# Optimization experiments

Hardware: AMD Instinct MI355X
Metric: run time of the kernel (lower is better)

Reference implementation:

```python
import jax, jax.numpy as jnp
import numpy as np

INPUT_SIZE = 695 + 2 * 406 + 84  # 1591
HIDDEN = 1024
NUM_LAYERS = 2
B, T = 8, 2048


def _make_linear(key, fan_in, fan_out, forget_bias):
    kw, kb = jax.random.split(key)
    bound = 1.0 / np.sqrt(fan_in)
    W = jax.random.uniform(kw, (fan_in, fan_out), minval=-bound, maxval=bound, dtype=jnp.float32)
    b = jax.random.uniform(kb, (fan_out,), minval=-bound, maxval=bound, dtype=jnp.float32)
    H = fan_out // 3
    b = b.at[H:2 * H].set(forget_bias)  # init_input_passthrough: forget-gate bias = 6.0
    return W, b


def setup_inputs() -> dict:
    key = jax.random.key(0)
    k1, k2, k3, k4, k5 = jax.random.split(key, 5)
    prev_actions = jax.random.uniform(k1, (B, T, 695), dtype=jnp.float32)
    states = jax.random.uniform(k2, (B, T, 812), dtype=jnp.float32)
    metadata = jax.random.uniform(k3, (B, T, 84), dtype=jnp.float32)
    W1, b1 = _make_linear(k4, INPUT_SIZE, 3 * HIDDEN, 6.0)
    W2, b2 = _make_linear(k5, HIDDEN, 3 * HIDDEN, 6.0)
    return {"prev_actions": prev_actions, "states": states, "metadata": metadata,
            "W1": W1, "b1": b1, "W2": W2, "b2": b2}


def forget_mult(f, z):
    # c_t = f_t * z_t + (1 - f_t) * c_{t-1}, c_0 = 0; parallel (log-depth) scan over time.
    a = 1.0 - f          # decay
    b = f * z            # input term
    def combine(c1, c2):
        a1, b1 = c1
        a2, b2 = c2
        return a1 * a2, a2 * b1 + b2
    _, c = jax.lax.associative_scan(combine, (a, b), axis=-2)
    return c


def qrnn_layer(x, W, b):
    y = jnp.einsum('btd,dh->bth', x, W) + b          # [B,T,3H]
    Z, Fg, O = jnp.split(y, 3, axis=-1)
    C = forget_mult(jax.nn.sigmoid(Fg), jax.nn.relu(Z))  # [B,T,H]
    out = jax.nn.sigmoid(O) * C
    return out, C[..., -1, :]


def reference(prev_actions, states, metadata, W1, b1, W2, b2):
    x = jnp.concatenate([prev_actions, states, metadata], axis=-1)  # [B,T,1591]
    hs = []
    for W, b in ((W1, b1), (W2, b2)):
        x, h_last = qrnn_layer(x, W, b)
        hs.append(h_last)
    h = jnp.stack(hs, axis=-2)  # [B, num_layers, H]
    return x, h
```

## Files before the change

kernel.cpp:

```cpp
#include <hip/hip_runtime.h>

typedef unsigned short u16;
typedef unsigned int   u32;
typedef __attribute__((ext_vector_type(8))) short bf16x8;
typedef __attribute__((ext_vector_type(4))) float f32x4;

#define B_ 8
#define T_ 2048
#define M_ 16384
#define N_ 3072
#define H_ 1024
#define L_ 64
#define NC_ 32

__device__ __forceinline__ u16 f2bf(float f) {
    union { float f; unsigned u; } v; v.f = f;
    unsigned r = v.u + 0x7FFFu + ((v.u >> 16) & 1u);
    return (u16)(r >> 16);
}
__device__ __forceinline__ float bf2f(u16 s) {
    union { unsigned u; float f; } v; v.u = ((unsigned)s) << 16;
    return v.f;
}
__device__ __forceinline__ float sigm(float x) {
    return 1.f / (1.f + __expf(-x));
}

__device__ __forceinline__ void gload_lds16(const void* g, void* l) {
    __builtin_amdgcn_global_load_lds(
        (const __attribute__((address_space(1))) unsigned int*)g,
        (__attribute__((address_space(3))) unsigned int*)l,
        16, 0, 0);
}

__global__ void concat_cast(const float* __restrict__ pa, const float* __restrict__ st,
                            const float* __restrict__ md, u16* __restrict__ x) {
    const int m = blockIdx.x;
    const float* pam = pa + (size_t)m * 695;
    const float* stm = st + (size_t)m * 812;
    const float* mdm = md + (size_t)m * 84;
    u16* xm = x + (size_t)m * 1600;
    for (int d = threadIdx.x; d < 1600; d += 256) {
        float v;
        if (d < 695)       v = pam[d];
        else if (d < 1507) v = stm[d - 695];
        else if (d < 1591) v = mdm[d - 1507];
        else               v = 0.f;
        xm[d] = f2bf(v);
    }
}

__global__ void wtrans(const float* __restrict__ W, u16* __restrict__ Wt, int K, int Kp) {
    __shared__ float tile[32][33];
    const int n0 = blockIdx.x << 5;
    const int k0 = blockIdx.y << 5;
    const int tx = threadIdx.x & 31, ty = threadIdx.x >> 5;
    #pragma unroll
    for (int i = 0; i < 32; i += 8) {
        int k = k0 + ty + i;
        tile[ty + i][tx] = (k < K) ? W[(size_t)k * N_ + n0 + tx] : 0.f;
    }
    __syncthreads();
    #pragma unroll
    for (int i = 0; i < 32; i += 8) {
        int n = n0 + ty + i;
        Wt[(size_t)n * Kp + k0 + tx] = f2bf(tile[tx][ty + i]);
    }
}

__global__ __launch_bounds__(256, 2)
void gemm_bt(const u16* __restrict__ A, const u16* __restrict__ Bt,
             const float* __restrict__ bias, u16* __restrict__ Y, int Kp) {
    __shared__ u16 a_tile[128 * 32];
    __shared__ u16 b_tile[128 * 32];
    const int tid = threadIdx.x;
    const int w = tid >> 6, l = tid & 63;
    const int brow = blockIdx.y << 7, bcol = blockIdx.x << 7;
    const int wr = (w >> 1) << 6, wc = (w & 1) << 6;
    const int lr = l & 15, lk = (l >> 4) << 3;

    const int ra0 = (w << 4) + (l >> 2);
    const int kc  = (l & 3) << 3;
    const u16* ga = A  + (size_t)(brow + ra0) * Kp + kc;
    const u16* gb = Bt + (size_t)(bcol + ra0) * Kp + kc;
    u16* la = a_tile + (w << 4) * 32;
    u16* lb = b_tile + (w << 4) * 32;

    f32x4 acc[4][4] = {};

    for (int kk = 0; kk < Kp; kk += 32) {
        gload_lds16(ga + kk,                    la);
        gload_lds16(ga + kk + (size_t)64 * Kp,  la + 64 * 32);
        gload_lds16(gb + kk,                    lb);
        gload_lds16(gb + kk + (size_t)64 * Kp,  lb + 64 * 32);
        __syncthreads();

        bf16x8 af[4], bfr[4];
        #pragma unroll
        for (int mi = 0; mi < 4; ++mi)
            af[mi] = *reinterpret_cast<const bf16x8*>(&a_tile[(wr + mi * 16 + lr) * 32 + lk]);
        #pragma unroll
        for (int ni = 0; ni < 4; ++ni)
            bfr[ni] = *reinterpret_cast<const bf16x8*>(&b_tile[(wc + ni * 16 + lr) * 32 + lk]);
        #pragma unroll
        for (int mi = 0; mi < 4; ++mi)
            #pragma unroll
            for (int ni = 0; ni < 4; ++ni)
                acc[mi][ni] = __builtin_amdgcn_mfma_f32_16x16x32_bf16(af[mi], bfr[ni], acc[mi][ni], 0, 0, 0);
        __syncthreads();
    }

    const int row0 = (l >> 4) << 2;
    #pragma unroll
    for (int ni = 0; ni < 4; ++ni) {
        const int gc = bcol + wc + ni * 16 + lr;
        const float bv = bias[gc];
        #pragma unroll
        for (int mi = 0; mi < 4; ++mi) {
            #pragma unroll
            for (int j = 0; j < 4; ++j) {
                const int gr = brow + wr + mi * 16 + row0 + j;
                Y[(size_t)gr * N_ + gc] = f2bf(acc[mi][ni][j] + bv);
            }
        }
    }
}

__global__ void scan_p1(const u16* __restrict__ y, float* __restrict__ aprod,
                        float* __restrict__ cend) {
    const int hb = blockIdx.x & 1;
    const int chunk = (blockIdx.x >> 1) & (NC_ - 1);
    const int b = blockIdx.x >> 6;
    const int h = (hb << 9) + (threadIdx.x << 1);
    const u16* yb = y + ((size_t)b * T_ + (size_t)chunk * L_) * N_;
    float a0 = 1.f, a1 = 1.f, c0 = 0.f, c1 = 0.f;
    #pragma unroll 4
    for (int t = 0; t < L_; ++t) {
        const u32 zz = *reinterpret_cast<const u32*>(&yb[t * N_ + h]);
        const u32 ff = *reinterpret_cast<const u32*>(&yb[t * N_ + H_ + h]);
        const float f0 = sigm(bf2f((u16)ff));
        const float f1 = sigm(bf2f((u16)(ff >> 16)));
        const float z0 = fmaxf(bf2f((u16)zz), 0.f);
        const float z1 = fmaxf(bf2f((u16)(zz >> 16)), 0.f);
        c0 = f0 * z0 + (1.f - f0) * c0;  a0 *= (1.f - f0);
        c1 = f1 * z1 + (1.f - f1) * c1;  a1 *= (1.f - f1);
    }
    const size_t idx = ((size_t)b * NC_ + chunk) * H_ + h;
    *reinterpret_cast<float2*>(&aprod[idx]) = make_float2(a0, a1);
    *reinterpret_cast<float2*>(&cend[idx])  = make_float2(c0, c1);
}

__global__ void scan_p2(const float* __restrict__ aprod, const float* __restrict__ cend,
                        float* __restrict__ cin, float* __restrict__ hout, int layer) {
    const int b = blockIdx.x >> 2;
    const int h = ((blockIdx.x & 3) << 8) + threadIdx.x;
    float c = 0.f;
    #pragma unroll
    for (int k = 0; k < NC_; ++k) {
        const size_t idx = ((size_t)b * NC_ + k) * H_ + h;
        cin[idx] = c;
        c = aprod[idx] * c + cend[idx];
    }
    hout[(size_t)(((b << 1) + layer) << 10) + h] = c;
}

__global__ void scan_p3(const u16* __restrict__ y, const float* __restrict__ cin,
                        void* __restrict__ xout, int layer) {
    const int hb = blockIdx.x & 1;
    const int chunk = (blockIdx.x >> 1) & (NC_ - 1);
    const int b = blockIdx.x >> 6;
    const int h = (hb << 9) + (threadIdx.x << 1);
    const u16* yb = y + ((size_t)b * T_ + (size_t)chunk * L_) * N_;
    const size_t cidx = ((size_t)b * NC_ + chunk) * H_ + h;
    const float2 cv = *reinterpret_cast<const float2*>(&cin[cidx]);
    float c0 = cv.x, c1 = cv.y;
    u32*    xo_bf = (u32*)xout;
    float2* xo_f  = (float2*)xout;
    const size_t obase = ((size_t)b * T_ + (size_t)chunk * L_) * H_ + h;
    #pragma unroll 4
    for (int t = 0; t < L_; ++t) {
        const u32 zz = *reinterpret_cast<const u32*>(&yb[t * N_ + h]);
        const u32 ff = *reinterpret_cast<const u32*>(&yb[t * N_ + H_ + h]);
        const u32 oo = *reinterpret_cast<const u32*>(&yb[t * N_ + 2 * H_ + h]);
        const float f0 = sigm(bf2f((u16)ff));
        const float f1 = sigm(bf2f((u16)(ff >> 16)));
        const float z0 = fmaxf(bf2f((u16)zz), 0.f);
        const float z1 = fmaxf(bf2f((u16)(zz >> 16)), 0.f);
        c0 = f0 * z0 + (1.f - f0) * c0;
        c1 = f1 * z1 + (1.f - f1) * c1;
        const float o0 = sigm(bf2f((u16)oo)) * c0;
        const float o1 = sigm(bf2f((u16)(oo >> 16))) * c1;
        const size_t oi = obase + (size_t)t * H_;
        if (layer) xo_f[oi >> 1] = make_float2(o0, o1);
        else       xo_bf[oi >> 1] = (u32)f2bf(o0) | ((u32)f2bf(o1) << 16);
    }
}

extern "C" void kernel_launch(void* const* d_in, const int* in_sizes, int n_in,
                              void* d_out, int out_size, void* d_ws, size_t ws_size,
                              hipStream_t stream) {
    const float* pa = (const float*)d_in[0];
    const float* st = (const float*)d_in[1];
    const float* md = (const float*)d_in[2];
    const float* W1 = (const float*)d_in[3];
    const float* b1 = (const float*)d_in[4];
    const float* W2 = (const float*)d_in[5];
    const float* b2 = (const float*)d_in[6];
    float* out = (float*)d_out;

    char* ws = (char*)d_ws;
    const size_t y_bytes = (size_t)M_ * N_ * 2;
    const size_t x_bytes = (size_t)M_ * 1600 * 2;
    u16* y  = (u16*)ws;
    u16* x  = (u16*)(ws + y_bytes);
    u16* Wt = (u16*)(ws + y_bytes + x_bytes);
    char* scr = ws + y_bytes + (size_t)M_ * H_ * 2;
    const size_t sarr = (size_t)B_ * NC_ * H_ * 4;
    float* aprod = (float*)scr;
    float* cend  = (float*)(scr + sarr);
    float* cin   = (float*)(scr + 2 * sarr);

    float* hout = out + (size_t)M_ * H_;

    concat_cast<<<M_, 256, 0, stream>>>(pa, st, md, x);
    wtrans<<<dim3(N_ / 32, 50), 256, 0, stream>>>(W1, Wt, 1591, 1600);
    gemm_bt<<<dim3(N_ / 128, M_ / 128), 256, 0, stream>>>(x, Wt, b1, y, 1600);
    scan_p1<<<B_ * NC_ * 2, 256, 0, stream>>>(y, aprod, cend);
    scan_p2<<<32, 256, 0, stream>>>(aprod, cend, cin, hout, 0);
    scan_p3<<<B_ * NC_ * 2, 256, 0, stream>>>(y, cin, x, 0);

    wtrans<<<dim3(N_ / 32, 32), 256, 0, stream>>>(W2, Wt, 1024, 1024);
    gemm_bt<<<dim3(N_ / 128, M_ / 128), 256, 0, stream>>>(x, Wt, b2, y, 1024);
    scan_p1<<<B_ * NC_ * 2, 256, 0, stream>>>(y, aprod, cend);
    scan_p2<<<32, 256, 0, stream>>>(aprod, cend, cin, hout, 1);
    scan_p3<<<B_ * NC_ * 2, 256, 0, stream>>>(y, cin, out, 1);
}
```

Measured before the change: 480.3 us.

## Replace GEMM with 256x256 8-wave ping-pong pipelined kernel with swizzled LDS

Replaces the 128x128 single-buffered bf16 MFMA GEMM with a 256x256-tile, 512-thread kernel. It double-buffers 64-wide K slices in 128KB of LDS, splits each K step into four phases that overlap global-to-LDS loads with MFMA work using explicit waitcnt, barriers and setprio, and XOR-swizzles LDS slots to avoid bank conflicts. Blocks are remapped across 8 groups (likely for XCD locality). The goal is more data reuse per tile and hidden memory latency. In exchange it runs one block per CU with heavy register use, and Kp=1600 must divide evenly into 64-wide K tiles (25 of them).

```diff
diff --git a/kernel.cpp b/kernel.cpp
--- a/kernel.cpp
+++ b/kernel.cpp
@@ -68,62 +68,108 @@
     }
 }
 
-__global__ __launch_bounds__(256, 2)
-void gemm_bt(const u16* __restrict__ A, const u16* __restrict__ Bt,
-             const float* __restrict__ bias, u16* __restrict__ Y, int Kp) {
-    __shared__ u16 a_tile[128 * 32];
-    __shared__ u16 b_tile[128 * 32];
+#define AO_(c, kh) ((((c) << 2) + (kh)) << 13)
+#define BO_(c, kh) ((((c) << 2) + 2 + (kh)) << 13)
+
+__global__ __launch_bounds__(512, 1)
+void gemm8p(const u16* __restrict__ A, const u16* __restrict__ Bt,
+            const float* __restrict__ bias, u16* __restrict__ Y,
+            int Kp, int NK, int NBN) {
+    __shared__ u16 lds[65536];
     const int tid = threadIdx.x;
     const int w = tid >> 6, l = tid & 63;
-    const int brow = blockIdx.y << 7, bcol = blockIdx.x << 7;
-    const int wr = (w >> 1) << 6, wc = (w & 1) << 6;
-    const int lr = l & 15, lk = (l >> 4) << 3;
-
-    const int ra0 = (w << 4) + (l >> 2);
-    const int kc  = (l & 3) << 3;
-    const u16* ga = A  + (size_t)(brow + ra0) * Kp + kc;
-    const u16* gb = Bt + (size_t)(bcol + ra0) * Kp + kc;
-    u16* la = a_tile + (w << 4) * 32;
-    u16* lb = b_tile + (w << 4) * 32;
-
-    f32x4 acc[4][4] = {};
-
-    for (int kk = 0; kk < Kp; kk += 32) {
-        gload_lds16(ga + kk,                    la);
-        gload_lds16(ga + kk + (size_t)64 * Kp,  la + 64 * 32);
-        gload_lds16(gb + kk,                    lb);
-        gload_lds16(gb + kk + (size_t)64 * Kp,  lb + 64 * 32);
-        __syncthreads();
-
-        bf16x8 af[4], bfr[4];
-        #pragma unroll
-        for (int mi = 0; mi < 4; ++mi)
-            af[mi] = *reinterpret_cast<const bf16x8*>(&a_tile[(wr + mi * 16 + lr) * 32 + lk]);
-        #pragma unroll
-        for (int ni = 0; ni < 4; ++ni)
-            bfr[ni] = *reinterpret_cast<const bf16x8*>(&b_tile[(wc + ni * 16 + lr) * 32 + lk]);
-        #pragma unroll
-        for (int mi = 0; mi < 4; ++mi)
-            #pragma unroll
-            for (int ni = 0; ni < 4; ++ni)
-                acc[mi][ni] = __builtin_amdgcn_mfma_f32_16x16x32_bf16(af[mi], bfr[ni], acc[mi][ni], 0, 0, 0);
-        __syncthreads();
-    }
-
-    const int row0 = (l >> 4) << 2;
-    #pragma unroll
-    for (int ni = 0; ni < 4; ++ni) {
-        const int gc = bcol + wc + ni * 16 + lr;
+    const int wm = w >> 2, wn = w & 3;
+
+    const int cpx = gridDim.x >> 3;
+    const int xg = (blockIdx.x & 7) * cpx + (blockIdx.x >> 3);
+    const int bm = xg / NBN, bn = xg % NBN;
+    const int brow = bm << 8, bcol = bn << 8;
+
+    const int srow = l >> 2;
+    const int gslot = (l & 3) ^ (srow & 3);
+    const u16* ga = A  + (size_t)(brow + w * 32 + srow) * Kp + gslot * 8;
+    const u16* gb = Bt + (size_t)(bcol + w * 32 + srow) * Kp + gslot * 8;
+    const int ldst = w << 10;
+
+    const int fl = ((l & 15) << 5) + ((((l >> 4) ^ (l & 3)) & 3) << 3);
+    const int abase0 = (wm << 7) << 5;
+    const int bbase0 = (wn << 6) << 5;
+
+#define STG(OFF, gp, kt, kh) do {                                              \
+    gload_lds16((gp) + (size_t)(kt) * 64 + (kh) * 32, &lds[(OFF) + ldst]);     \
+    gload_lds16((gp) + 16 * (size_t)Kp + (size_t)(kt) * 64 + (kh) * 32,        \
+                &lds[(OFF) + ldst + 512]);                                     \
+} while (0)
+
+    f32x4 acc[8][4] = {};
+    bf16x8 bfr[4];
+
+    STG(AO_(0, 0), ga, 0, 0); STG(BO_(0, 0), gb, 0, 0);
+    STG(AO_(0, 1), ga, 0, 1); STG(BO_(0, 1), gb, 0, 1);
+    STG(AO_(1, 0), ga, 1, 0); STG(BO_(1, 0), gb, 1, 0);
+    asm volatile("s_waitcnt vmcnt(4)" ::: "memory");
+    __builtin_amdgcn_s_barrier();
+    asm volatile("" ::: "memory");
+
+#define PHASE(CH, KH, LOADB, STAGECODE, VMW) do {                              \
+    bf16x8 af[4];                                                              \
+    { const int ab = AO_(cur, KH) + abase0 + ((CH) << 11);                     \
+      _Pragma("unroll")                                                        \
+      for (int mf = 0; mf < 4; ++mf)                                           \
+          af[mf] = *reinterpret_cast<const bf16x8*>(&lds[ab + (mf << 9) + fl]);\
+    }                                                                          \
+    if (LOADB) {                                                               \
+        const int bb = BO_(cur, KH) + bbase0;                                  \
+        _Pragma("unroll")                                                      \
+        for (int nf = 0; nf < 4; ++nf)                                         \
+            bfr[nf] = *reinterpret_cast<const bf16x8*>(&lds[bb + (nf << 9) + fl]); \
+    }                                                                          \
+    STAGECODE;                                                                 \
+    if (VMW) asm volatile("s_waitcnt vmcnt(4)" ::: "memory");                  \
+    asm volatile("" ::: "memory");                                             \
+    __builtin_amdgcn_s_barrier();                                              \
+    asm volatile("s_waitcnt lgkmcnt(0)" ::: "memory");                         \
+    __builtin_amdgcn_sched_barrier(0);                                         \
+    __builtin_amdgcn_s_setprio(1);                                             \
+    _Pragma("unroll")                                                          \
+    for (int mf = 0; mf < 4; ++mf)                                             \
+        _Pragma("unroll")                                                      \
+        for (int nf = 0; nf < 4; ++nf)                                         \
+            acc[(CH) * 4 + mf][nf] = __builtin_amdgcn_mfma_f32_16x16x32_bf16(  \
+                af[mf], bfr[nf], acc[(CH) * 4 + mf][nf], 0, 0, 0);             \
+    __builtin_amdgcn_s_setprio(0);                                             \
+    __builtin_amdgcn_sched_barrier(0);                                         \
+    __builtin_amdgcn_s_barrier();                                              \
+    asm volatile("" ::: "memory");                                             \
+} while (0)
+
+    for (int kt = 0; kt < NK; ++kt) {
+        const int cur = kt & 1;
+        const int kn1 = (kt + 1 < NK) ? kt + 1 : kt;
+        const int kn2 = (kt + 2 < NK) ? kt + 2 : kt;
+        PHASE(0, 0, 1, { STG(AO_(cur ^ 1, 1), ga, kn1, 1); }, 0);
+        PHASE(1, 0, 0, { STG(BO_(cur ^ 1, 1), gb, kn1, 1); }, 1);
+        PHASE(0, 1, 1, { STG(AO_(cur, 0),     ga, kn2, 0); }, 0);
+        PHASE(1, 1, 0, { STG(BO_(cur, 0),     gb, kn2, 0); }, 1);
+    }
+
+    asm volatile("s_waitcnt vmcnt(0)" ::: "memory");
+
+    const int crow0 = brow + wm * 128 + ((l >> 4) << 2);
+    const int ccol0 = bcol + wn * 64 + (l & 15);
+    #pragma unroll
+    for (int nf = 0; nf < 4; ++nf) {
+        const int gc = ccol0 + nf * 16;
         const float bv = bias[gc];
         #pragma unroll
-        for (int mi = 0; mi < 4; ++mi) {
+        for (int mfi = 0; mfi < 8; ++mfi) {
             #pragma unroll
-            for (int j = 0; j < 4; ++j) {
-                const int gr = brow + wr + mi * 16 + row0 + j;
-                Y[(size_t)gr * N_ + gc] = f2bf(acc[mi][ni][j] + bv);
-            }
+            for (int j = 0; j < 4; ++j)
+                Y[(size_t)(crow0 + mfi * 16 + j) * N_ + gc] = f2bf(acc[mfi][nf][j] + bv);
         }
     }
+#undef PHASE
+#undef STG
 }
 
 __global__ void scan_p1(const u16* __restrict__ y, float* __restrict__ aprod,
@@ -222,15 +268,17 @@
 
     float* hout = out + (size_t)M_ * H_;
 
+    const int grid_g = (M_ / 256) * (N_ / 256);
+
     concat_cast<<<M_, 256, 0, stream>>>(pa, st, md, x);
     wtrans<<<dim3(N_ / 32, 50), 256, 0, stream>>>(W1, Wt, 1591, 1600);
-    gemm_bt<<<dim3(N_ / 128, M_ / 128), 256, 0, stream>>>(x, Wt, b1, y, 1600);
+    gemm8p<<<grid_g, 512, 0, stream>>>(x, Wt, b1, y, 1600, 25, N_ / 256);
     scan_p1<<<B_ * NC_ * 2, 256, 0, stream>>>(y, aprod, cend);
     scan_p2<<<32, 256, 0, stream>>>(aprod, cend, cin, hout, 0);
     scan_p3<<<B_ * NC_ * 2, 256, 0, stream>>>(y, cin, x, 0);
 
     wtrans<<<dim3(N_ / 32, 32), 256, 0, stream>>>(W2, Wt, 1024, 1024);
-    gemm_bt<<<dim3(N_ / 128, M_ / 128), 256, 0, stream>>>(x, Wt, b2, y, 1024);
+    gemm8p<<<grid_g, 512, 0, stream>>>(x, Wt, b2, y, 1024, 16, N_ / 256);
     scan_p1<<<B_ * NC_ * 2, 256, 0, stream>>>(y, aprod, cend);
     scan_p2<<<32, 256, 0, stream>>>(aprod, cend, cin, hout, 1);
     scan_p3<<<B_ * NC_ * 2, 256, 0, stream>>>(y, cin, out, 1);
```

Measured after the change: 455.1 us. -5.2%, faster.

## Rewrite GEMM with 256x128 tiles, triple-buffered LDS prefetch, swizzle, coalesced epilogue

Applied to the files above, without the earlier changes.

Replaces the simple double-sync GEMM with a 256x128 block tile. Global-to-LDS loads are triple-buffered two k-steps ahead with manual waitcnt and one barrier per iteration. LDS layouts are XOR-swizzled to avoid bank conflicts, blocks are remapped across XCDs, and the output is staged through LDS so it can be written with 16-byte coalesced stores. The concat/cast kernel also packs two bf16 values per store. The trade-off is higher register and LDS use (72KB) and hand-written synchronisation that must be exactly right.

```diff
diff --git a/kernel.cpp b/kernel.cpp
--- a/kernel.cpp
+++ b/kernel.cpp
@@ -4,6 +4,7 @@
 typedef unsigned int   u32;
 typedef __attribute__((ext_vector_type(8))) short bf16x8;
 typedef __attribute__((ext_vector_type(4))) float f32x4;
+typedef __attribute__((ext_vector_type(2))) unsigned int u32x2;
 
 #define B_ 8
 #define T_ 2048
@@ -33,20 +34,24 @@
         16, 0, 0);
 }
 
+__device__ __forceinline__ float cc_el(int d, const float* pam, const float* stm,
+                                       const float* mdm) {
+    if (d < 695)  return pam[d];
+    if (d < 1507) return stm[d - 695];
+    if (d < 1591) return mdm[d - 1507];
+    return 0.f;
+}
 __global__ void concat_cast(const float* __restrict__ pa, const float* __restrict__ st,
                             const float* __restrict__ md, u16* __restrict__ x) {
     const int m = blockIdx.x;
     const float* pam = pa + (size_t)m * 695;
     const float* stm = st + (size_t)m * 812;
     const float* mdm = md + (size_t)m * 84;
-    u16* xm = x + (size_t)m * 1600;
-    for (int d = threadIdx.x; d < 1600; d += 256) {
-        float v;
-        if (d < 695)       v = pam[d];
-        else if (d < 1507) v = stm[d - 695];
-        else if (d < 1591) v = mdm[d - 1507];
-        else               v = 0.f;
-        xm[d] = f2bf(v);
+    u32* xm = (u32*)(x + (size_t)m * 1600);
+    for (int d2 = threadIdx.x; d2 < 800; d2 += 256) {
+        const float v0 = cc_el(d2 * 2,     pam, stm, mdm);
+        const float v1 = cc_el(d2 * 2 + 1, pam, stm, mdm);
+        xm[d2] = (u32)f2bf(v0) | ((u32)f2bf(v1) << 16);
     }
 }
 
@@ -69,61 +74,113 @@
 }
 
 __global__ __launch_bounds__(256, 2)
-void gemm_bt(const u16* __restrict__ A, const u16* __restrict__ Bt,
-             const float* __restrict__ bias, u16* __restrict__ Y, int Kp) {
-    __shared__ u16 a_tile[128 * 32];
-    __shared__ u16 b_tile[128 * 32];
+void gemm8p(const u16* __restrict__ A, const u16* __restrict__ Bt,
+            const float* __restrict__ bias, u16* __restrict__ Y,
+            int Kp, int NK, int NBN) {
+    __shared__ u16 lds[36864];
     const int tid = threadIdx.x;
     const int w = tid >> 6, l = tid & 63;
-    const int brow = blockIdx.y << 7, bcol = blockIdx.x << 7;
-    const int wr = (w >> 1) << 6, wc = (w & 1) << 6;
-    const int lr = l & 15, lk = (l >> 4) << 3;
-
-    const int ra0 = (w << 4) + (l >> 2);
-    const int kc  = (l & 3) << 3;
-    const u16* ga = A  + (size_t)(brow + ra0) * Kp + kc;
-    const u16* gb = Bt + (size_t)(bcol + ra0) * Kp + kc;
-    u16* la = a_tile + (w << 4) * 32;
-    u16* lb = b_tile + (w << 4) * 32;
-
-    f32x4 acc[4][4] = {};
-
-    for (int kk = 0; kk < Kp; kk += 32) {
-        gload_lds16(ga + kk,                    la);
-        gload_lds16(ga + kk + (size_t)64 * Kp,  la + 64 * 32);
-        gload_lds16(gb + kk,                    lb);
-        gload_lds16(gb + kk + (size_t)64 * Kp,  lb + 64 * 32);
-        __syncthreads();
-
-        bf16x8 af[4], bfr[4];
-        #pragma unroll
-        for (int mi = 0; mi < 4; ++mi)
-            af[mi] = *reinterpret_cast<const bf16x8*>(&a_tile[(wr + mi * 16 + lr) * 32 + lk]);
-        #pragma unroll
-        for (int ni = 0; ni < 4; ++ni)
-            bfr[ni] = *reinterpret_cast<const bf16x8*>(&b_tile[(wc + ni * 16 + lr) * 32 + lk]);
-        #pragma unroll
-        for (int mi = 0; mi < 4; ++mi)
+    const int wm = w >> 1, wn = w & 1;
+
+    const int cpx = gridDim.x >> 3;
+    const int xg = (blockIdx.x & 7) * cpx + (blockIdx.x >> 3);
+    const int bm = xg / NBN, bn = xg % NBN;
+    const int brow = bm << 8, bcol = bn << 7;
+
+    const int gslot = (l & 3) ^ ((l >> 3) & 3);
+    const u16* pA = A  + (size_t)(brow + (w << 4) + (l >> 2)) * Kp + gslot * 8;
+    const u16* pB = Bt + (size_t)(bcol + (w << 4) + (l >> 2)) * Kp + gslot * 8;
+
+#define STG_A(r, kt) do {                                                           \
+    gload_lds16(pA + (size_t)(kt) * 32,                    &lds[(r) * 12288 + (w << 9)]);        \
+    gload_lds16(pA + (size_t)(kt) * 32 +  64 * (size_t)Kp, &lds[(r) * 12288 + 2048 + (w << 9)]); \
+    gload_lds16(pA + (size_t)(kt) * 32 + 128 * (size_t)Kp, &lds[(r) * 12288 + 4096 + (w << 9)]); \
+    gload_lds16(pA + (size_t)(kt) * 32 + 192 * (size_t)Kp, &lds[(r) * 12288 + 6144 + (w << 9)]); \
+} while (0)
+#define STG_B(r, kt) do {                                                           \
+    gload_lds16(pB + (size_t)(kt) * 32,                   &lds[(r) * 12288 + 8192 + (w << 9)]);         \
+    gload_lds16(pB + (size_t)(kt) * 32 + 64 * (size_t)Kp, &lds[(r) * 12288 + 8192 + 2048 + (w << 9)]);  \
+} while (0)
+
+    const int fl = ((l & 15) << 5) + ((((l >> 4) ^ ((l >> 1) & 3)) & 3) << 3);
+    const int abase = wm << 12;
+    const int bbase = 8192 + (wn << 11);
+
+    f32x4 acc[8][4] = {};
+
+    STG_A(0, 0); STG_B(0, 0);
+    STG_A(1, 1); STG_B(1, 1);
+    asm volatile("s_waitcnt vmcnt(6)" ::: "memory");
+    __builtin_amdgcn_s_barrier();
+    asm volatile("" ::: "memory");
+
+    for (int kt = 0; kt < NK; ++kt) {
+        const int cur = kt % 3;
+        const int nb  = (kt + 2) % 3;
+        const int nxt = (kt + 2 < NK) ? kt + 2 : kt;
+        STG_A(nb, nxt); STG_B(nb, nxt);
+
+        bf16x8 afr[8], bfr[4];
+        const int cb = cur * 12288;
+        #pragma unroll
+        for (int mf = 0; mf < 8; ++mf)
+            afr[mf] = *reinterpret_cast<const bf16x8*>(&lds[cb + abase + (mf << 9) + fl]);
+        #pragma unroll
+        for (int nf = 0; nf < 4; ++nf)
+            bfr[nf] = *reinterpret_cast<const bf16x8*>(&lds[cb + bbase + (nf << 9) + fl]);
+
+        __builtin_amdgcn_s_setprio(1);
+        #pragma unroll
+        for (int mf = 0; mf < 8; ++mf)
             #pragma unroll
-            for (int ni = 0; ni < 4; ++ni)
-                acc[mi][ni] = __builtin_amdgcn_mfma_f32_16x16x32_bf16(af[mi], bfr[ni], acc[mi][ni], 0, 0, 0);
-        __syncthreads();
-    }
-
-    const int row0 = (l >> 4) << 2;
-    #pragma unroll
-    for (int ni = 0; ni < 4; ++ni) {
-        const int gc = bcol + wc + ni * 16 + lr;
-        const float bv = bias[gc];
-        #pragma unroll
-        for (int mi = 0; mi < 4; ++mi) {
-            #pragma unroll
-            for (int j = 0; j < 4; ++j) {
-                const int gr = brow + wr + mi * 16 + row0 + j;
-                Y[(size_t)gr * N_ + gc] = f2bf(acc[mi][ni][j] + bv);
-            }
+            for (int nf = 0; nf < 4; ++nf)
+                acc[mf][nf] = __builtin_amdgcn_mfma_f32_16x16x32_bf16(
+                    bfr[nf], afr[mf], acc[mf][nf], 0, 0, 0);
+        __builtin_amdgcn_s_setprio(0);
+
+        asm volatile("s_waitcnt vmcnt(6)" ::: "memory");
+        asm volatile("s_waitcnt lgkmcnt(0)" ::: "memory");
+        __builtin_amdgcn_s_barrier();
+        asm volatile("" ::: "memory");
+    }
+
+    asm volatile("s_waitcnt vmcnt(0)" ::: "memory");
+    __builtin_amdgcn_s_barrier();
+
+    const int nq = (l >> 4) << 2;
+    float4 bv4[4];
+    #pragma unroll
+    for (int nf = 0; nf < 4; ++nf)
+        bv4[nf] = *reinterpret_cast<const float4*>(&bias[bcol + (wn << 6) + nf * 16 + nq]);
+    #pragma unroll
+    for (int mf = 0; mf < 8; ++mf) {
+        const int mrow = (wm << 7) + (mf << 4) + (l & 15);
+        #pragma unroll
+        for (int nf = 0; nf < 4; ++nf) {
+            const int nloc = (wn << 6) + nf * 16 + nq;
+            u32x2 p;
+            p.x = (u32)f2bf(acc[mf][nf][0] + bv4[nf].x) |
+                  ((u32)f2bf(acc[mf][nf][1] + bv4[nf].y) << 16);
+            p.y = (u32)f2bf(acc[mf][nf][2] + bv4[nf].z) |
+                  ((u32)f2bf(acc[mf][nf][3] + bv4[nf].w) << 16);
+            const int idx16 = (nloc >> 3) ^ ((mrow & 7) << 1);
+            const int boff = (mrow << 8) + (idx16 << 4) + ((nloc >> 2) & 1) * 8;
+            *reinterpret_cast<u32x2*>(&((char*)lds)[boff]) = p;
         }
     }
+    asm volatile("s_waitcnt lgkmcnt(0)" ::: "memory");
+    __builtin_amdgcn_s_barrier();
+
+    #pragma unroll
+    for (int ip = 0; ip < 16; ++ip) {
+        const int mrow = (w << 6) + (ip << 2) + (l >> 4);
+        const int idx16 = (l & 15) ^ ((mrow & 7) << 1);
+        const bf16x8 v = *reinterpret_cast<const bf16x8*>(
+            &((char*)lds)[(mrow << 8) + (idx16 << 4)]);
+        *reinterpret_cast<bf16x8*>(&Y[(size_t)(brow + mrow) * N_ + bcol + (l & 15) * 8]) = v;
+    }
+#undef STG_A
+#undef STG_B
 }
 
 __global__ void scan_p1(const u16* __restrict__ y, float* __restrict__ aprod,
@@ -222,15 +279,17 @@
 
     float* hout = out + (size_t)M_ * H_;
 
+    const int grid_g = (M_ / 256) * (N_ / 128);
+
     concat_cast<<<M_, 256, 0, stream>>>(pa, st, md, x);
     wtrans<<<dim3(N_ / 32, 50), 256, 0, stream>>>(W1, Wt, 1591, 1600);
-    gemm_bt<<<dim3(N_ / 128, M_ / 128), 256, 0, stream>>>(x, Wt, b1, y, 1600);
+    gemm8p<<<grid_g, 256, 0, stream>>>(x, Wt, b1, y, 1600, 50, N_ / 128);
     scan_p1<<<B_ * NC_ * 2, 256, 0, stream>>>(y, aprod, cend);
     scan_p2<<<32, 256, 0, stream>>>(aprod, cend, cin, hout, 0);
     scan_p3<<<B_ * NC_ * 2, 256, 0, stream>>>(y, cin, x, 0);
 
     wtrans<<<dim3(N_ / 32, 32), 256, 0, stream>>>(W2, Wt, 1024, 1024);
-    gemm_bt<<<dim3(N_ / 128, M_ / 128), 256, 0, stream>>>(x, Wt, b2, y, 1024);
+    gemm8p<<<grid_g, 256, 0, stream>>>(x, Wt, b2, y, 1024, 32, N_ / 128);
     scan_p1<<<B_ * NC_ * 2, 256, 0, stream>>>(y, aprod, cend);
     scan_p2<<<32, 256, 0, stream>>>(aprod, cend, cin, hout, 1);
     scan_p3<<<B_ * NC_ * 2, 256, 0, stream>>>(y, cin, out, 1);
```

New measurement: 430.7 us. 1.12x faster.
